# Kernel tuning notes

Hardware: AMD Instinct MI355X
Metric: run time of the kernel (lower is better)

## Reference

```python
import jax, jax.numpy as jnp
from jax import lax
import numpy as np

# ChannelMamba (bimamba_type='v2') from Wave-MambaAD VSSBlock.
# Dims: b=4, d_model=256 (channel dim of u), h=w=64 -> l=h*w=4096=dim,
# expand=1 -> d_inner=256, d_state=16, dt_rank=ceil(256/16)=16.
B_, DM, H_, W_ = 4, 256, 64, 64
L_ = H_ * W_            # == init arg `dim` (LayerNorm + depthwise-conv channels)
DI = DM                 # d_inner = expand * d_model
N_ = 16                 # d_state
R_ = 16                 # dt_rank


def setup_inputs() -> dict:
    key = jax.random.key(0)
    ks = jax.random.split(key, 12)
    s = 0.05
    # dt_proj bias init exactly as in the module: inv-softplus of dt in [1e-3, 1e-1]
    rs = np.random.RandomState(0)
    dt = np.exp(rs.rand(DI) * (np.log(0.1) - np.log(0.001)) + np.log(0.001))
    dt = np.clip(dt, 1e-4, None)
    inv_dt = dt + np.log1p(-np.exp(-dt))
    A_log = jnp.log(jnp.tile(jnp.arange(1, N_ + 1, dtype=jnp.float32), (DI, 1)))
    return {
        "u": jax.random.normal(ks[0], (B_, DM, H_, W_), jnp.float32),
        "in_proj_w": jax.random.normal(ks[1], (2 * DI, DM), jnp.float32) * s,
        "conv_w": jax.random.normal(ks[2], (L_, 1, 3, 3), jnp.float32) * s,  # depthwise, groups=L_
        "conv_b": jnp.zeros((L_,), jnp.float32),
        "x_proj_w": jax.random.normal(ks[3], (R_ + 2 * N_, DI), jnp.float32) * s,
        "dt_proj_w": jax.random.normal(ks[4], (DI, R_), jnp.float32) * (R_ ** -0.5),
        "dt_bias": jnp.asarray(inv_dt, jnp.float32),
        "A_log": A_log,
        "D": jnp.ones((DI,), jnp.float32),
        "x_proj_b_w": jax.random.normal(ks[5], (R_ + 2 * N_, DI), jnp.float32) * s,
        "dt_proj_b_w": jax.random.normal(ks[6], (DI, R_), jnp.float32) * (R_ ** -0.5),
        "A_b_log": A_log,
        "D_b": jnp.ones((DI,), jnp.float32),
        "ln_w": jnp.ones((L_,), jnp.float32),
        "ln_b": jnp.zeros((L_,), jnp.float32),
        "ln1_w": jnp.ones((L_,), jnp.float32),
        "ln1_b": jnp.zeros((L_,), jnp.float32),
    }


def _layernorm(x, w, b, eps=1e-5):
    m = jnp.mean(x, axis=-1, keepdims=True)
    v = jnp.mean(jnp.square(x - m), axis=-1, keepdims=True)
    return (x - m) * lax.rsqrt(v + eps) * w + b


def _selective_scan(u, delta, A, Bm, Cm, D, z, delta_bias):
    # u, delta, z: (b,d,l); A: (d,n); Bm, Cm: (b,n,l); D, delta_bias: (d,)
    delta = jax.nn.softplus(delta + delta_bias[None, :, None])
    dT = jnp.transpose(delta, (2, 0, 1))  # (l,b,d)
    uT = jnp.transpose(u, (2, 0, 1))      # (l,b,d)
    BT = jnp.transpose(Bm, (2, 0, 1))     # (l,b,n)
    CT = jnp.transpose(Cm, (2, 0, 1))     # (l,b,n)

    def step(hcar, inp):
        d_t, u_t, B_t, C_t = inp
        dA = jnp.exp(d_t[:, :, None] * A)                       # (b,d,n)
        hcar = hcar * dA + (d_t * u_t)[:, :, None] * B_t[:, None, :]
        y_t = jnp.einsum('bdn,bn->bd', hcar, C_t)
        return hcar, y_t

    h0 = jnp.zeros((u.shape[0], u.shape[1], A.shape[1]), u.dtype)
    _, ys = lax.scan(step, h0, (dT, uT, BT, CT))                 # ys: (l,b,d)
    y = jnp.transpose(ys, (1, 2, 0)) + D[None, :, None] * u      # (b,d,l)
    return y * jax.nn.silu(z)                                    # internal z-gate of selective_scan_fn


def reference(u, in_proj_w, conv_w, conv_b, x_proj_w, dt_proj_w, dt_bias, A_log, D,
              x_proj_b_w, dt_proj_b_w, A_b_log, D_b, ln_w, ln_b, ln1_w, ln1_b):
    b, d, h, w = u.shape
    l = h * w
    r = dt_proj_w.shape[1]
    n = A_log.shape[1]
    u_bld = u.reshape(b, d, l).transpose(0, 2, 1)                # (b,l,d)
    xz = jnp.einsum('ed,bld->bel', in_proj_w, u_bld)             # (b,2*d_inner,l), no bias
    x, z = jnp.split(xz, 2, axis=1)                              # each (b,d_inner,l)

    # depthwise 3x3 conv: channels = l, spatial = (1, d_inner), padding 1 (no activation!)
    xc = x.transpose(0, 2, 1)[:, :, None, :]                     # (b,l,1,d_inner)
    xc = lax.conv_general_dilated(xc, conv_w, (1, 1), ((1, 1), (1, 1)),
                                  feature_group_count=l,
                                  dimension_numbers=('NCHW', 'OIHW', 'NCHW'))
    x = (xc + conv_b[None, :, None, None])[:, :, 0, :].transpose(0, 2, 1)  # (b,d_inner,l)

    def proj(xp_w, dtp_w):
        dbl = jnp.einsum('kd,bdl->bkl', xp_w, x)                 # (b,r+2n,l)
        dt = jnp.einsum('dr,brl->bdl', dtp_w, dbl[:, :r])        # (b,d_inner,l), no bias here
        return dt, dbl[:, r:r + n], dbl[:, r + n:]               # dt, B, C

    A = -jnp.exp(A_log)
    A_b = -jnp.exp(A_b_log)
    dt, Bm, Cm = proj(x_proj_w, dt_proj_w)
    dtb, Bb, Cb = proj(x_proj_b_w, dt_proj_b_w)

    y = _selective_scan(x, dt, A, Bm, Cm, D, z, dt_bias)
    # backward scan: flipped input; NOTE: module uses forward dt_bias and unflipped z here
    yb = _selective_scan(x[:, :, ::-1], dtb, A_b, Bb, Cb, D_b, z, dt_bias)

    out = _layernorm(y, ln_w, ln_b) * jax.nn.silu(z)
    out_b = _layernorm(yb, ln1_w, ln1_b) * jax.nn.silu(z)
    return (out + out_b[:, :, ::-1]).reshape(b, d, h, w)
```

## Files before the change

kernel.cpp:

```cpp
#include <hip/hip_runtime.h>
#include <math.h>

#define BN 4
#define DD 256
#define LL 4096
#define NS 16
#define NCH 128
#define CT 32
#define SROW 36
#define BROW 20
#define LOG2E 1.4426950408889634f

typedef __bf16 bf16x8 __attribute__((ext_vector_type(8)));
typedef float f32x4 __attribute__((ext_vector_type(4)));

__device__ __forceinline__ float softplus_f(float v) {
  float e = __builtin_amdgcn_exp2f(v * LOG2E);
  float r = 0.69314718056f * __builtin_amdgcn_logf(1.f + e);
  return v > 20.f ? v : r;
}
__device__ __forceinline__ float silu_f(float v) {
  return v / (1.f + __expf(-v));
}
__device__ __forceinline__ f32x4 exp2v(f32x4 a) {
  f32x4 r;
  r[0] = __builtin_amdgcn_exp2f(a[0]);
  r[1] = __builtin_amdgcn_exp2f(a[1]);
  r[2] = __builtin_amdgcn_exp2f(a[2]);
  r[3] = __builtin_amdgcn_exp2f(a[3]);
  return r;
}

__global__ __launch_bounds__(256) void k1_mfma(
    const float* __restrict__ W, const float* __restrict__ u,
    float* __restrict__ xpre, float* __restrict__ zb) {
  __shared__ float Af[128 * 36];
  __shared__ float Bf[32 * 68];
  const int l0 = blockIdx.x * 64;
  const int e0 = blockIdx.y * 128;
  const int b  = blockIdx.z;
  const int tid = threadIdx.x;
  const int lane = tid & 63, w = tid >> 6;
  const int m16 = lane & 15, quad = lane >> 4;

  f32x4 acc[2][4];
#pragma unroll
  for (int i = 0; i < 2; ++i)
#pragma unroll
    for (int j = 0; j < 4; ++j) acc[i][j] = (f32x4){0.f, 0.f, 0.f, 0.f};

  const float* Ub = u + (size_t)b * DD * LL;

  for (int k0 = 0; k0 < DD; k0 += 32) {
    if (k0) __syncthreads();
#pragma unroll
    for (int it = 0; it < 4; ++it) {
      int f4 = tid + it * 256;
      int e = f4 >> 3, kq = f4 & 7;
      *(float4*)&Af[e * 36 + kq * 4] =
          *(const float4*)(W + (size_t)(e0 + e) * DD + k0 + kq * 4);
    }
#pragma unroll
    for (int it = 0; it < 2; ++it) {
      int f4 = tid + it * 256;
      int kk = f4 >> 4, lq = f4 & 15;
      *(float4*)&Bf[kk * 68 + lq * 4] =
          *(const float4*)(Ub + (size_t)(k0 + kk) * LL + l0 + lq * 4);
    }
    __syncthreads();
    bf16x8 afr[2], bfr[4];
#pragma unroll
    for (int te = 0; te < 2; ++te) {
      const float* src = &Af[(w * 32 + te * 16 + m16) * 36 + quad * 8];
      bf16x8 t;
#pragma unroll
      for (int j = 0; j < 8; ++j) t[j] = (__bf16)src[j];
      afr[te] = t;
    }
#pragma unroll
    for (int tl = 0; tl < 4; ++tl) {
      bf16x8 t;
#pragma unroll
      for (int j = 0; j < 8; ++j) t[j] = (__bf16)Bf[(quad * 8 + j) * 68 + tl * 16 + m16];
      bfr[tl] = t;
    }
#pragma unroll
    for (int te = 0; te < 2; ++te)
#pragma unroll
      for (int tl = 0; tl < 4; ++tl)
        acc[te][tl] = __builtin_amdgcn_mfma_f32_16x16x32_bf16(afr[te], bfr[tl], acc[te][tl], 0, 0, 0);
  }

#pragma unroll
  for (int te = 0; te < 2; ++te) {
#pragma unroll
    for (int tl = 0; tl < 4; ++tl) {
      int col = l0 + tl * 16 + m16;
#pragma unroll
      for (int r = 0; r < 4; ++r) {
        int e = e0 + w * 32 + te * 16 + quad * 4 + r;
        float v = acc[te][tl][r];
        if (e < DD) xpre[((size_t)b * DD + e) * LL + col] = v;
        else        zb[((size_t)b * DD + (e - DD)) * LL + col] = v;
      }
    }
  }
}

__global__ __launch_bounds__(256) void k2_conv(
    const float* __restrict__ xpre, const float* __restrict__ cw,
    const float* __restrict__ cb, float* __restrict__ xo) {
  const int bd = blockIdx.x;
  const int d = bd & 255;
  const size_t row = (size_t)bd * LL;
  const float* r1 = xpre + row;
  const bool has0 = d > 0, has2 = d < DD - 1;
  for (int j = threadIdx.x; j < LL; j += 256) {
    float w0 = cw[j * 9 + 3], w1 = cw[j * 9 + 4], w2 = cw[j * 9 + 5];
    float v = cb[j] + r1[j] * w1;
    if (has0) v += r1[j - LL] * w0;
    if (has2) v += r1[j + LL] * w2;
    xo[row + j] = v;
  }
}

__global__ __launch_bounds__(256) void k3_xproj(
    const float* __restrict__ xc,
    const float* __restrict__ xpw, const float* __restrict__ xpwB,
    float* __restrict__ dtr, float* __restrict__ gB, float* __restrict__ gC) {
  const int tid = threadIdx.x;
  const int l   = blockIdx.x * 256 + tid;
  const int b   = blockIdx.y;
  const int zz  = blockIdx.z;
  const int dir = zz >> 3, rg = zz & 7;
  const int rbase = rg * 6;
  const float* W = (dir ? xpwB : xpw) + (size_t)rbase * DD;
  const float* xcol = xc + (size_t)b * DD * LL + l;

  float acc[6] = {0.f, 0.f, 0.f, 0.f, 0.f, 0.f};

#pragma unroll 8
  for (int d = 0; d < DD; ++d) {
    float xv = xcol[(size_t)d * LL];
#pragma unroll
    for (int i = 0; i < 6; ++i) acc[i] += W[i * DD + d] * xv;
  }

  const size_t ob = ((size_t)dir * BN + b);
#pragma unroll
  for (int i = 0; i < 6; ++i) {
    int r = rbase + i;
    if (r < 16)
      dtr[(ob * 16 + r) * LL + l] = acc[i];
    else if (r < 32)
      gB[(ob * NS + (r - 16)) * LL + l] = acc[i];
    else
      gC[(ob * NS + (r - 32)) * LL + l] = acc[i];
  }
}

__global__ __launch_bounds__(256) void k3b_dtproj(
    const float* __restrict__ dtr,
    const float* __restrict__ dtw, const float* __restrict__ dtwB,
    const float* __restrict__ dtb,
    float* __restrict__ gdelta) {
  const int tid = threadIdx.x;
  const int l   = blockIdx.x * 256 + tid;
  const int b   = blockIdx.y & 3;
  const int dir = blockIdx.y >> 2;
  const int d0  = blockIdx.z * 16;
  const size_t ob = ((size_t)dir * BN + b);
  const float* dw = (dir ? dtwB : dtw);

  float tr[16];
#pragma unroll
  for (int r = 0; r < 16; ++r) tr[r] = dtr[(ob * 16 + r) * LL + l];

#pragma unroll
  for (int d = d0; d < d0 + 16; ++d) {
    float acc = dtb[d];
#pragma unroll
    for (int r = 0; r < 16; ++r) acc += dw[d * 16 + r] * tr[r];
    gdelta[(ob * DD + d) * LL + l] = softplus_f(acc);
  }
}

__global__ __launch_bounds__(256) void k4_scanA(
    const float* __restrict__ gdelta, const float* __restrict__ x,
    const float* __restrict__ gB,
    const float* __restrict__ Alog, const float* __restrict__ AlogB,
    float* __restrict__ Pbuf, float* __restrict__ qbuf) {
  __shared__ float sdl[64 * SROW];
  __shared__ float sx[64 * SROW];
  __shared__ float sB[CT * BROW];
  const int s = blockIdx.x;
  const int d0 = blockIdx.y * 64;
  const int dir = blockIdx.z >> 2, b = blockIdx.z & 3;
  const int t0 = s * CT;
  const int tid = threadIdx.x;
  const size_t ob = (size_t)dir * BN + b;

  {
    const int q = tid & 7, r2 = tid >> 3;
#pragma unroll
    for (int p = 0; p < 2; ++p) {
      int row = r2 + p * 32;
      f32x4 dl = *(const f32x4*)(gdelta + (ob * DD + d0 + row) * LL + t0 + q * 4);
      f32x4 xv;
      if (dir == 0) {
        xv = *(const f32x4*)(x + ((size_t)b * DD + d0 + row) * LL + t0 + q * 4);
      } else {
        f32x4 t = *(const f32x4*)(x + ((size_t)b * DD + d0 + row) * LL + (LL - 4 - t0 - q * 4));
        xv = (f32x4){t[3], t[2], t[1], t[0]};
      }
      *(f32x4*)&sdl[row * SROW + q * 4] = dl;
      *(f32x4*)&sx[row * SROW + q * 4] = xv;
    }
    const int t = tid & 31, n8 = tid >> 5;
#pragma unroll
    for (int p = 0; p < 2; ++p) {
      int n = n8 + p * 8;
      sB[t * BROW + n] = gB[(ob * NS + n) * LL + t0 + t];
    }
  }
  __syncthreads();

  const int dq = tid >> 2, sub = tid & 3, n0 = sub * 4;
  const int d = d0 + dq;
  f32x4 Al = *(const f32x4*)((dir ? AlogB : Alog) + d * NS + n0);
  f32x4 An2;
  An2[0] = -__expf(Al[0]) * LOG2E;
  An2[1] = -__expf(Al[1]) * LOG2E;
  An2[2] = -__expf(Al[2]) * LOG2E;
  An2[3] = -__expf(Al[3]) * LOG2E;

  f32x4 h = (f32x4){0.f, 0.f, 0.f, 0.f};
  float S = 0.f;

  for (int jb = 0; jb < CT; jb += 4) {
    f32x4 dl4 = *(const f32x4*)&sdl[dq * SROW + jb];
    f32x4 x4  = *(const f32x4*)&sx[dq * SROW + jb];
#pragma unroll
    for (int q = 0; q < 4; ++q) {
      int t = jb + q;
      f32x4 Bv = *(const f32x4*)&sB[t * BROW + n0];
      float dl = dl4[q];
      float dlx = dl * x4[q];
      f32x4 e = exp2v(dl * An2);
      h = h * e + dlx * Bv;
      S += dl;
    }
  }

  const size_t pidx = ((ob * DD + d) * (size_t)NCH + s) * NS + n0;
  *(f32x4*)(Pbuf + pidx) = exp2v(An2 * S);
  *(f32x4*)(qbuf + pidx) = h;
}

__global__ __launch_bounds__(64) void k5_mid(
    const float* __restrict__ Pbuf, float* __restrict__ qbuf) {
  int id = blockIdx.x * 64 + threadIdx.x;
  int n = id & 15;
  int d = (id >> 4) & 255;
  int rb = id >> 12;
  size_t base = (((size_t)rb * DD + d) * NCH) * NS + n;
  float h = 0.f;
  for (int s0 = 0; s0 < NCH; s0 += 8) {
    float Pv[8], qv[8];
#pragma unroll
    for (int k = 0; k < 8; ++k) {
      size_t idx = base + (size_t)(s0 + k) * NS;
      Pv[k] = Pbuf[idx];
      qv[k] = qbuf[idx];
    }
#pragma unroll
    for (int k = 0; k < 8; ++k) {
      size_t idx = base + (size_t)(s0 + k) * NS;
      qbuf[idx] = h;
      h = h * Pv[k] + qv[k];
    }
  }
}

__global__ __launch_bounds__(256) void k6_scanC(
    const float* __restrict__ gdelta, const float* __restrict__ x,
    const float* __restrict__ gB, const float* __restrict__ gC,
    const float* __restrict__ zb,
    const float* __restrict__ Alog, const float* __restrict__ AlogB,
    const float* __restrict__ Dvec, const float* __restrict__ DvecB,
    const float* __restrict__ hstart,
    float* __restrict__ y, float* __restrict__ yb) {
  __shared__ float sdl[64 * SROW];
  __shared__ float sx[64 * SROW];
  __shared__ float sB[CT * BROW];
  __shared__ float sC[CT * BROW];
  __shared__ float ylds[64 * 36];
  __shared__ float sD[64];
  const int s = blockIdx.x;
  const int d0 = blockIdx.y * 64;
  const int dir = blockIdx.z >> 2, b = blockIdx.z & 3;
  const int t0 = s * CT;
  const int tid = threadIdx.x;
  const size_t ob = (size_t)dir * BN + b;

  {
    const int q = tid & 7, r2 = tid >> 3;
#pragma unroll
    for (int p = 0; p < 2; ++p) {
      int row = r2 + p * 32;
      f32x4 dl = *(const f32x4*)(gdelta + (ob * DD + d0 + row) * LL + t0 + q * 4);
      f32x4 xv;
      if (dir == 0) {
        xv = *(const f32x4*)(x + ((size_t)b * DD + d0 + row) * LL + t0 + q * 4);
      } else {
        f32x4 t = *(const f32x4*)(x + ((size_t)b * DD + d0 + row) * LL + (LL - 4 - t0 - q * 4));
        xv = (f32x4){t[3], t[2], t[1], t[0]};
      }
      *(f32x4*)&sdl[row * SROW + q * 4] = dl;
      *(f32x4*)&sx[row * SROW + q * 4] = xv;
    }
    const int t = tid & 31, n8 = tid >> 5;
#pragma unroll
    for (int p = 0; p < 2; ++p) {
      int n = n8 + p * 8;
      sB[t * BROW + n] = gB[(ob * NS + n) * LL + t0 + t];
      sC[t * BROW + n] = gC[(ob * NS + n) * LL + t0 + t];
    }
    if (tid < 64) sD[tid] = (dir ? DvecB : Dvec)[d0 + tid];
  }
  __syncthreads();

  const int dq = tid >> 2, sub = tid & 3, n0 = sub * 4;
  const int lane = tid & 63, w = tid >> 6;
  const int d = d0 + dq;
  f32x4 Al = *(const f32x4*)((dir ? AlogB : Alog) + d * NS + n0);
  f32x4 An2;
  An2[0] = -__expf(Al[0]) * LOG2E;
  An2[1] = -__expf(Al[1]) * LOG2E;
  An2[2] = -__expf(Al[2]) * LOG2E;
  An2[3] = -__expf(Al[3]) * LOG2E;

  const size_t pidx = ((ob * DD + d) * (size_t)NCH + s) * NS + n0;
  f32x4 h = *(const f32x4*)(hstart + pidx);

  const float* zbase = zb + ((size_t)b * DD + d0) * LL + t0;
  float* dbase = (dir ? yb : y) + ((size_t)b * DD + d0) * LL + t0;
  const int dql = lane >> 3, tql = lane & 7;

  for (int jb = 0; jb < CT; jb += 8) {
#pragma unroll
    for (int j2 = 0; j2 < 8; j2 += 4) {
      f32x4 dl4 = *(const f32x4*)&sdl[dq * SROW + jb + j2];
      f32x4 x4  = *(const f32x4*)&sx[dq * SROW + jb + j2];
#pragma unroll
      for (int q = 0; q < 4; ++q) {
        int t = jb + j2 + q;
        f32x4 Bv = *(const f32x4*)&sB[t * BROW + n0];
        f32x4 Cv = *(const f32x4*)&sC[t * BROW + n0];
        float dl = dl4[q];
        float dlx = dl * x4[q];
        f32x4 e = exp2v(dl * An2);
        h = h * e + dlx * Bv;
        f32x4 yc = h * Cv;
        ylds[dq * 36 + ((j2 + q) << 2) + sub] = (yc[0] + yc[1]) + (yc[2] + yc[3]);
      }
    }
#pragma unroll
    for (int k = 0; k < 2; ++k) {
      int dd = w * 16 + dql + 8 * k;
      int tt = jb + tql;
      f32x4 pv = *(const f32x4*)&ylds[dd * 36 + tql * 4];
      float sum = (pv[0] + pv[1]) + (pv[2] + pv[3]);
      float xv = sx[dd * SROW + tt];
      float zv = zbase[(size_t)dd * LL + tt];
      dbase[(size_t)dd * LL + tt] = (sum + sD[dd] * xv) * silu_f(zv);
    }
  }
}

__global__ __launch_bounds__(256) void k7_final(
    const float* __restrict__ y, const float* __restrict__ yb,
    const float* __restrict__ zb,
    const float* __restrict__ lnw, const float* __restrict__ lnb,
    const float* __restrict__ ln1w, const float* __restrict__ ln1b,
    float* __restrict__ out) {
  __shared__ float sy[LL];
  __shared__ float syb[LL];
  __shared__ float rsum[4][4];
  const int row = blockIdx.x;
  const int tid = threadIdx.x;
  const size_t base = (size_t)row * LL;
  float s1y = 0.f, s2y = 0.f, s1b = 0.f, s2b = 0.f;
  for (int j = tid * 4; j < LL; j += 1024) {
    float4 v = *(const float4*)(y + base + j);
    *(float4*)&sy[j] = v;
    s1y += v.x + v.y + v.z + v.w;
    s2y += v.x * v.x + v.y * v.y + v.z * v.z + v.w * v.w;
    float4 w = *(const float4*)(yb + base + j);
    *(float4*)&syb[j] = w;
    s1b += w.x + w.y + w.z + w.w;
    s2b += w.x * w.x + w.y * w.y + w.z * w.z + w.w * w.w;
  }
#pragma unroll
  for (int m = 1; m < 64; m <<= 1) {
    s1y += __shfl_xor(s1y, m); s2y += __shfl_xor(s2y, m);
    s1b += __shfl_xor(s1b, m); s2b += __shfl_xor(s2b, m);
  }
  int wv = tid >> 6;
  if ((tid & 63) == 0) { rsum[wv][0] = s1y; rsum[wv][1] = s2y; rsum[wv][2] = s1b; rsum[wv][3] = s2b; }
  __syncthreads();
  float t1y = rsum[0][0] + rsum[1][0] + rsum[2][0] + rsum[3][0];
  float t2y = rsum[0][1] + rsum[1][1] + rsum[2][1] + rsum[3][1];
  float t1b = rsum[0][2] + rsum[1][2] + rsum[2][2] + rsum[3][2];
  float t2b = rsum[0][3] + rsum[1][3] + rsum[2][3] + rsum[3][3];
  const float inv = 1.f / (float)LL;
  float mY = t1y * inv; float vY = t2y * inv - mY * mY; float rY = rsqrtf(vY + 1e-5f);
  float mB = t1b * inv; float vB = t2b * inv - mB * mB; float rB = rsqrtf(vB + 1e-5f);
  for (int j = tid; j < LL; j += 256) {
    int jr = LL - 1 - j;
    float a  = (sy[j]  - mY) * rY * lnw[j]   + lnb[j];
    float g1 = silu_f(zb[base + j]);
    float bv = (syb[jr] - mB) * rB * ln1w[jr] + ln1b[jr];
    float g2 = silu_f(zb[base + jr]);
    out[base + j] = a * g1 + bv * g2;
  }
}

extern "C" void kernel_launch(void* const* d_in, const int* in_sizes, int n_in,
                              void* d_out, int out_size, void* d_ws, size_t ws_size,
                              hipStream_t stream) {
  const float* u     = (const float*)d_in[0];
  const float* inw   = (const float*)d_in[1];
  const float* cw    = (const float*)d_in[2];
  const float* cb    = (const float*)d_in[3];
  const float* xpw   = (const float*)d_in[4];
  const float* dtw   = (const float*)d_in[5];
  const float* dtb   = (const float*)d_in[6];
  const float* Alog  = (const float*)d_in[7];
  const float* Dv    = (const float*)d_in[8];
  const float* xpwB  = (const float*)d_in[9];
  const float* dtwB  = (const float*)d_in[10];
  const float* AlogB = (const float*)d_in[11];
  const float* DvB   = (const float*)d_in[12];
  const float* lnw   = (const float*)d_in[13];
  const float* lnb   = (const float*)d_in[14];
  const float* ln1w  = (const float*)d_in[15];
  const float* ln1b  = (const float*)d_in[16];
  float* out = (float*)d_out;

  float* ws = (float*)d_ws;
  const size_t SZ = (size_t)BN * DD * LL;
  float* xpre   = ws;
  float* zb     = ws + SZ;
  float* xc     = ws + 2 * SZ;
  float* gdelta = ws + 3 * SZ;
  float* gB     = ws + 5 * SZ;
  float* gC     = gB + SZ / 8;
  float* Pbuf   = gC + SZ / 8;
  float* qbuf   = Pbuf + SZ;
  float* ybuf   = xpre;
  float* ybbuf  = Pbuf;
  float* dtr    = Pbuf;

  k1_mfma<<<dim3(64, 4, 4), 256, 0, stream>>>(inw, u, xpre, zb);
  k2_conv<<<1024, 256, 0, stream>>>(xpre, cw, cb, xc);
  k3_xproj<<<dim3(16, 4, 16), 256, 0, stream>>>(xc, xpw, xpwB, dtr, gB, gC);
  k3b_dtproj<<<dim3(16, 8, 16), 256, 0, stream>>>(dtr, dtw, dtwB, dtb, gdelta);
  k4_scanA<<<dim3(NCH - 1, 4, 8), 256, 0, stream>>>(gdelta, xc, gB, Alog, AlogB, Pbuf, qbuf);
  k5_mid<<<512, 64, 0, stream>>>(Pbuf, qbuf);
  k6_scanC<<<dim3(NCH, 4, 8), 256, 0, stream>>>(gdelta, xc, gB, gC, zb, Alog, AlogB,
                                                Dv, DvB, qbuf, ybuf, ybbuf);
  k7_final<<<1024, 256, 0, stream>>>(ybuf, ybbuf, zb, lnw, lnb, ln1w, ln1b, out);
}
```

Measured before the change: 245.3 us.

## Read scan inputs directly from global memory, store chunk delta sums, reduce via DPP

The chunked scan kernels no longer stage delta and x rows through shared memory. Each thread reads its own row straight from global memory, with the 4 threads of a quad reading the same addresses. Scan-A now writes one scalar delta sum per chunk instead of 16 decay factors, and the middle pass recomputes the decay with exp2. Scan-C replaces the LDS-based y reduction with a DPP quad reduction and has each thread write 8 contiguous outputs, which removes shared-memory traffic and barriers. The cost is redundant global/L1 loads across a quad and extra exp work in the middle pass.

New measurement: 259.5 us. +5.8%, slower.

```diff
diff --git a/kernel.cpp b/kernel.cpp
--- a/kernel.cpp
+++ b/kernel.cpp
@@ -7,7 +7,6 @@
 #define NS 16
 #define NCH 128
 #define CT 32
-#define SROW 36
 #define BROW 20
 #define LOG2E 1.4426950408889634f
 
@@ -29,6 +28,12 @@
   r[2] = __builtin_amdgcn_exp2f(a[2]);
   r[3] = __builtin_amdgcn_exp2f(a[3]);
   return r;
+}
+__device__ __forceinline__ float quad_reduce(float v) {
+  int t = __builtin_amdgcn_mov_dpp(__float_as_int(v), 0xB1, 0xF, 0xF, true);
+  v += __int_as_float(t);
+  t = __builtin_amdgcn_mov_dpp(__float_as_int(v), 0x4E, 0xF, 0xF, true);
+  return v + __int_as_float(t);
 }
 
 __global__ __launch_bounds__(256) void k1_mfma(
@@ -189,10 +194,8 @@
     const float* __restrict__ gdelta, const float* __restrict__ x,
     const float* __restrict__ gB,
     const float* __restrict__ Alog, const float* __restrict__ AlogB,
-    float* __restrict__ Pbuf, float* __restrict__ qbuf) {
-  __shared__ float sdl[64 * SROW];
-  __shared__ float sx[64 * SROW];
-  __shared__ float sB[CT * BROW];
+    float* __restrict__ Sbuf, float* __restrict__ qbuf) {
+  __shared__ __align__(16) float sB[CT * BROW];
   const int s = blockIdx.x;
   const int d0 = blockIdx.y * 64;
   const int dir = blockIdx.z >> 2, b = blockIdx.z & 3;
@@ -201,21 +204,6 @@
   const size_t ob = (size_t)dir * BN + b;
 
   {
-    const int q = tid & 7, r2 = tid >> 3;
-#pragma unroll
-    for (int p = 0; p < 2; ++p) {
-      int row = r2 + p * 32;
-      f32x4 dl = *(const f32x4*)(gdelta + (ob * DD + d0 + row) * LL + t0 + q * 4);
-      f32x4 xv;
-      if (dir == 0) {
-        xv = *(const f32x4*)(x + ((size_t)b * DD + d0 + row) * LL + t0 + q * 4);
-      } else {
-        f32x4 t = *(const f32x4*)(x + ((size_t)b * DD + d0 + row) * LL + (LL - 4 - t0 - q * 4));
-        xv = (f32x4){t[3], t[2], t[1], t[0]};
-      }
-      *(f32x4*)&sdl[row * SROW + q * 4] = dl;
-      *(f32x4*)&sx[row * SROW + q * 4] = xv;
-    }
     const int t = tid & 31, n8 = tid >> 5;
 #pragma unroll
     for (int p = 0; p < 2; ++p) {
@@ -234,12 +222,21 @@
   An2[2] = -__expf(Al[2]) * LOG2E;
   An2[3] = -__expf(Al[3]) * LOG2E;
 
+  const float* dlrow = gdelta + (ob * DD + d) * LL + t0;
+  const float* xrow  = x + ((size_t)b * DD + d) * LL;
+
   f32x4 h = (f32x4){0.f, 0.f, 0.f, 0.f};
   float S = 0.f;
 
   for (int jb = 0; jb < CT; jb += 4) {
-    f32x4 dl4 = *(const f32x4*)&sdl[dq * SROW + jb];
-    f32x4 x4  = *(const f32x4*)&sx[dq * SROW + jb];
+    f32x4 dl4 = *(const f32x4*)(dlrow + jb);
+    f32x4 x4;
+    if (dir == 0) {
+      x4 = *(const f32x4*)(xrow + t0 + jb);
+    } else {
+      f32x4 t = *(const f32x4*)(xrow + (LL - 4 - t0 - jb));
+      x4 = (f32x4){t[3], t[2], t[1], t[0]};
+    }
 #pragma unroll
     for (int q = 0; q < 4; ++q) {
       int t = jb + q;
@@ -252,32 +249,36 @@
     }
   }
 
+  if (sub == 0) Sbuf[(ob * DD + d) * (size_t)NCH + s] = S;
   const size_t pidx = ((ob * DD + d) * (size_t)NCH + s) * NS + n0;
-  *(f32x4*)(Pbuf + pidx) = exp2v(An2 * S);
   *(f32x4*)(qbuf + pidx) = h;
 }
 
 __global__ __launch_bounds__(64) void k5_mid(
-    const float* __restrict__ Pbuf, float* __restrict__ qbuf) {
+    const float* __restrict__ Sbuf,
+    const float* __restrict__ Alog, const float* __restrict__ AlogB,
+    float* __restrict__ qbuf) {
   int id = blockIdx.x * 64 + threadIdx.x;
   int n = id & 15;
   int d = (id >> 4) & 255;
   int rb = id >> 12;
+  int dir = rb >> 2;
+  float An2 = -__expf((dir ? AlogB : Alog)[d * NS + n]) * LOG2E;
   size_t base = (((size_t)rb * DD + d) * NCH) * NS + n;
+  size_t sbase = ((size_t)rb * DD + d) * NCH;
   float h = 0.f;
   for (int s0 = 0; s0 < NCH; s0 += 8) {
-    float Pv[8], qv[8];
+    float Sv[8], qv[8];
 #pragma unroll
     for (int k = 0; k < 8; ++k) {
-      size_t idx = base + (size_t)(s0 + k) * NS;
-      Pv[k] = Pbuf[idx];
-      qv[k] = qbuf[idx];
+      Sv[k] = Sbuf[sbase + s0 + k];
+      qv[k] = qbuf[base + (size_t)(s0 + k) * NS];
     }
 #pragma unroll
     for (int k = 0; k < 8; ++k) {
       size_t idx = base + (size_t)(s0 + k) * NS;
       qbuf[idx] = h;
-      h = h * Pv[k] + qv[k];
+      h = h * __builtin_amdgcn_exp2f(An2 * Sv[k]) + qv[k];
     }
   }
 }
@@ -290,12 +291,8 @@
     const float* __restrict__ Dvec, const float* __restrict__ DvecB,
     const float* __restrict__ hstart,
     float* __restrict__ y, float* __restrict__ yb) {
-  __shared__ float sdl[64 * SROW];
-  __shared__ float sx[64 * SROW];
-  __shared__ float sB[CT * BROW];
-  __shared__ float sC[CT * BROW];
-  __shared__ float ylds[64 * 36];
-  __shared__ float sD[64];
+  __shared__ __align__(16) float sB[CT * BROW];
+  __shared__ __align__(16) float sC[CT * BROW];
   const int s = blockIdx.x;
   const int d0 = blockIdx.y * 64;
   const int dir = blockIdx.z >> 2, b = blockIdx.z & 3;
@@ -304,21 +301,6 @@
   const size_t ob = (size_t)dir * BN + b;
 
   {
-    const int q = tid & 7, r2 = tid >> 3;
-#pragma unroll
-    for (int p = 0; p < 2; ++p) {
-      int row = r2 + p * 32;
-      f32x4 dl = *(const f32x4*)(gdelta + (ob * DD + d0 + row) * LL + t0 + q * 4);
-      f32x4 xv;
-      if (dir == 0) {
-        xv = *(const f32x4*)(x + ((size_t)b * DD + d0 + row) * LL + t0 + q * 4);
-      } else {
-        f32x4 t = *(const f32x4*)(x + ((size_t)b * DD + d0 + row) * LL + (LL - 4 - t0 - q * 4));
-        xv = (f32x4){t[3], t[2], t[1], t[0]};
-      }
-      *(f32x4*)&sdl[row * SROW + q * 4] = dl;
-      *(f32x4*)&sx[row * SROW + q * 4] = xv;
-    }
     const int t = tid & 31, n8 = tid >> 5;
 #pragma unroll
     for (int p = 0; p < 2; ++p) {
@@ -326,12 +308,10 @@
       sB[t * BROW + n] = gB[(ob * NS + n) * LL + t0 + t];
       sC[t * BROW + n] = gC[(ob * NS + n) * LL + t0 + t];
     }
-    if (tid < 64) sD[tid] = (dir ? DvecB : Dvec)[d0 + tid];
   }
   __syncthreads();
 
   const int dq = tid >> 2, sub = tid & 3, n0 = sub * 4;
-  const int lane = tid & 63, w = tid >> 6;
   const int d = d0 + dq;
   f32x4 Al = *(const f32x4*)((dir ? AlogB : Alog) + d * NS + n0);
   f32x4 An2;
@@ -339,43 +319,60 @@
   An2[1] = -__expf(Al[1]) * LOG2E;
   An2[2] = -__expf(Al[2]) * LOG2E;
   An2[3] = -__expf(Al[3]) * LOG2E;
+  const float Dd = (dir ? DvecB : Dvec)[d];
 
   const size_t pidx = ((ob * DD + d) * (size_t)NCH + s) * NS + n0;
   f32x4 h = *(const f32x4*)(hstart + pidx);
 
-  const float* zbase = zb + ((size_t)b * DD + d0) * LL + t0;
-  float* dbase = (dir ? yb : y) + ((size_t)b * DD + d0) * LL + t0;
-  const int dql = lane >> 3, tql = lane & 7;
+  const float* dlrow = gdelta + (ob * DD + d) * LL + t0;
+  const float* xrow  = x + ((size_t)b * DD + d) * LL;
+
+  float yreg[8], xreg[8];
 
   for (int jb = 0; jb < CT; jb += 8) {
-#pragma unroll
-    for (int j2 = 0; j2 < 8; j2 += 4) {
-      f32x4 dl4 = *(const f32x4*)&sdl[dq * SROW + jb + j2];
-      f32x4 x4  = *(const f32x4*)&sx[dq * SROW + jb + j2];
-#pragma unroll
-      for (int q = 0; q < 4; ++q) {
-        int t = jb + j2 + q;
-        f32x4 Bv = *(const f32x4*)&sB[t * BROW + n0];
-        f32x4 Cv = *(const f32x4*)&sC[t * BROW + n0];
-        float dl = dl4[q];
-        float dlx = dl * x4[q];
-        f32x4 e = exp2v(dl * An2);
-        h = h * e + dlx * Bv;
-        f32x4 yc = h * Cv;
-        ylds[dq * 36 + ((j2 + q) << 2) + sub] = (yc[0] + yc[1]) + (yc[2] + yc[3]);
-      }
-    }
-#pragma unroll
-    for (int k = 0; k < 2; ++k) {
-      int dd = w * 16 + dql + 8 * k;
-      int tt = jb + tql;
-      f32x4 pv = *(const f32x4*)&ylds[dd * 36 + tql * 4];
-      float sum = (pv[0] + pv[1]) + (pv[2] + pv[3]);
-      float xv = sx[dd * SROW + tt];
-      float zv = zbase[(size_t)dd * LL + tt];
-      dbase[(size_t)dd * LL + tt] = (sum + sD[dd] * xv) * silu_f(zv);
-    }
-  }
+    f32x4 dlA = *(const f32x4*)(dlrow + jb);
+    f32x4 dlB = *(const f32x4*)(dlrow + jb + 4);
+    f32x4 xA, xB;
+    if (dir == 0) {
+      xA = *(const f32x4*)(xrow + t0 + jb);
+      xB = *(const f32x4*)(xrow + t0 + jb + 4);
+    } else {
+      f32x4 ta = *(const f32x4*)(xrow + (LL - 4 - t0 - jb));
+      f32x4 tb = *(const f32x4*)(xrow + (LL - 4 - t0 - (jb + 4)));
+      xA = (f32x4){ta[3], ta[2], ta[1], ta[0]};
+      xB = (f32x4){tb[3], tb[2], tb[1], tb[0]};
+    }
+    const bool own = (sub == (jb >> 3));
+#pragma unroll
+    for (int tl = 0; tl < 8; ++tl) {
+      float dl = tl < 4 ? dlA[tl & 3] : dlB[tl & 3];
+      float xv = tl < 4 ? xA[tl & 3] : xB[tl & 3];
+      int t = jb + tl;
+      f32x4 Bv = *(const f32x4*)&sB[t * BROW + n0];
+      f32x4 Cv = *(const f32x4*)&sC[t * BROW + n0];
+      float dlx = dl * xv;
+      f32x4 e = exp2v(dl * An2);
+      h = h * e + dlx * Bv;
+      f32x4 yc = h * Cv;
+      float part = (yc[0] + yc[1]) + (yc[2] + yc[3]);
+      float sum = quad_reduce(part);
+      yreg[tl] = own ? sum : yreg[tl];
+      xreg[tl] = own ? xv : xreg[tl];
+    }
+  }
+
+  const size_t rbase = ((size_t)b * DD + d) * LL + t0 + sub * 8;
+  f32x4 z0 = *(const f32x4*)(zb + rbase);
+  f32x4 z1 = *(const f32x4*)(zb + rbase + 4);
+  float* dst = (dir ? yb : y) + rbase;
+  f32x4 o0, o1;
+#pragma unroll
+  for (int i = 0; i < 4; ++i) {
+    o0[i] = (yreg[i] + Dd * xreg[i]) * silu_f(z0[i]);
+    o1[i] = (yreg[i + 4] + Dd * xreg[i + 4]) * silu_f(z1[i]);
+  }
+  *(f32x4*)dst = o0;
+  *(f32x4*)(dst + 4) = o1;
 }
 
 __global__ __launch_bounds__(256) void k7_final(
@@ -456,18 +453,19 @@
   float* gdelta = ws + 3 * SZ;
   float* gB     = ws + 5 * SZ;
   float* gC     = gB + SZ / 8;
-  float* Pbuf   = gC + SZ / 8;
-  float* qbuf   = Pbuf + SZ;
+  float* Pregion= gC + SZ / 8;
+  float* qbuf   = Pregion + SZ;
+  float* Sbuf   = Pregion;
   float* ybuf   = xpre;
-  float* ybbuf  = Pbuf;
-  float* dtr    = Pbuf;
+  float* ybbuf  = Pregion;
+  float* dtr    = Pregion;
 
   k1_mfma<<<dim3(64, 4, 4), 256, 0, stream>>>(inw, u, xpre, zb);
   k2_conv<<<1024, 256, 0, stream>>>(xpre, cw, cb, xc);
   k3_xproj<<<dim3(16, 4, 16), 256, 0, stream>>>(xc, xpw, xpwB, dtr, gB, gC);
   k3b_dtproj<<<dim3(16, 8, 16), 256, 0, stream>>>(dtr, dtw, dtwB, dtb, gdelta);
-  k4_scanA<<<dim3(NCH - 1, 4, 8), 256, 0, stream>>>(gdelta, xc, gB, Alog, AlogB, Pbuf, qbuf);
-  k5_mid<<<512, 64, 0, stream>>>(Pbuf, qbuf);
+  k4_scanA<<<dim3(NCH - 1, 4, 8), 256, 0, stream>>>(gdelta, xc, gB, Alog, AlogB, Sbuf, qbuf);
+  k5_mid<<<512, 64, 0, stream>>>(Sbuf, Alog, AlogB, qbuf);
   k6_scanC<<<dim3(NCH, 4, 8), 256, 0, stream>>>(gdelta, xc, gB, gC, zb, Alog, AlogB,
                                                 Dv, DvB, qbuf, ybuf, ybbuf);
   k7_final<<<1024, 256, 0, stream>>>(ybuf, ybbuf, zb, lnw, lnb, ln1w, ln1b, out);
```

## Keep scan inputs in registers and reduce outputs with DPP in k6

Applied to the files above, without the earlier changes.

The chunked scan-output kernel no longer stages delta and x through shared memory. Each thread loads its own 32-step row into registers, reduces the partial y across the four state-group lanes with DPP quad shuffles instead of an LDS transpose, and writes eight contiguous outputs as vector stores. This removes most LDS traffic and the ylds round trip, and turns the scattered z and y accesses into coalesced vector accesses. In exchange it raises register pressure, and the four lanes of a quad issue redundant loads of the same delta and x row.

New measurement: 253.6 us. +3.4%, slower.

```diff
diff --git a/kernel.cpp b/kernel.cpp
--- a/kernel.cpp
+++ b/kernel.cpp
@@ -29,6 +29,12 @@
   r[2] = __builtin_amdgcn_exp2f(a[2]);
   r[3] = __builtin_amdgcn_exp2f(a[3]);
   return r;
+}
+__device__ __forceinline__ float quad_reduce(float v) {
+  int t = __builtin_amdgcn_mov_dpp(__float_as_int(v), 0xB1, 0xF, 0xF, true);
+  v += __int_as_float(t);
+  t = __builtin_amdgcn_mov_dpp(__float_as_int(v), 0x4E, 0xF, 0xF, true);
+  return v + __int_as_float(t);
 }
 
 __global__ __launch_bounds__(256) void k1_mfma(
@@ -290,12 +296,8 @@
     const float* __restrict__ Dvec, const float* __restrict__ DvecB,
     const float* __restrict__ hstart,
     float* __restrict__ y, float* __restrict__ yb) {
-  __shared__ float sdl[64 * SROW];
-  __shared__ float sx[64 * SROW];
-  __shared__ float sB[CT * BROW];
-  __shared__ float sC[CT * BROW];
-  __shared__ float ylds[64 * 36];
-  __shared__ float sD[64];
+  __shared__ __align__(16) float sB[CT * BROW];
+  __shared__ __align__(16) float sC[CT * BROW];
   const int s = blockIdx.x;
   const int d0 = blockIdx.y * 64;
   const int dir = blockIdx.z >> 2, b = blockIdx.z & 3;
@@ -304,21 +306,6 @@
   const size_t ob = (size_t)dir * BN + b;
 
   {
-    const int q = tid & 7, r2 = tid >> 3;
-#pragma unroll
-    for (int p = 0; p < 2; ++p) {
-      int row = r2 + p * 32;
-      f32x4 dl = *(const f32x4*)(gdelta + (ob * DD + d0 + row) * LL + t0 + q * 4);
-      f32x4 xv;
-      if (dir == 0) {
-        xv = *(const f32x4*)(x + ((size_t)b * DD + d0 + row) * LL + t0 + q * 4);
-      } else {
-        f32x4 t = *(const f32x4*)(x + ((size_t)b * DD + d0 + row) * LL + (LL - 4 - t0 - q * 4));
-        xv = (f32x4){t[3], t[2], t[1], t[0]};
-      }
-      *(f32x4*)&sdl[row * SROW + q * 4] = dl;
-      *(f32x4*)&sx[row * SROW + q * 4] = xv;
-    }
     const int t = tid & 31, n8 = tid >> 5;
 #pragma unroll
     for (int p = 0; p < 2; ++p) {
@@ -326,56 +313,80 @@
       sB[t * BROW + n] = gB[(ob * NS + n) * LL + t0 + t];
       sC[t * BROW + n] = gC[(ob * NS + n) * LL + t0 + t];
     }
-    if (tid < 64) sD[tid] = (dir ? DvecB : Dvec)[d0 + tid];
-  }
-  __syncthreads();
+  }
 
   const int dq = tid >> 2, sub = tid & 3, n0 = sub * 4;
-  const int lane = tid & 63, w = tid >> 6;
   const int d = d0 + dq;
+  const float* dlrow = gdelta + (ob * DD + d) * LL + t0;
+  const float* xrow  = x + ((size_t)b * DD + d) * LL;
+
+  f32x4 dlv[8], xv[8];
+#pragma unroll
+  for (int i = 0; i < 8; ++i) {
+    dlv[i] = *(const f32x4*)(dlrow + i * 4);
+    if (dir == 0) {
+      xv[i] = *(const f32x4*)(xrow + t0 + i * 4);
+    } else {
+      f32x4 t = *(const f32x4*)(xrow + (LL - 4 - t0 - i * 4));
+      xv[i] = (f32x4){t[3], t[2], t[1], t[0]};
+    }
+  }
+  const size_t pidx = ((ob * DD + d) * (size_t)NCH + s) * NS + n0;
+  f32x4 h = *(const f32x4*)(hstart + pidx);
+
   f32x4 Al = *(const f32x4*)((dir ? AlogB : Alog) + d * NS + n0);
   f32x4 An2;
   An2[0] = -__expf(Al[0]) * LOG2E;
   An2[1] = -__expf(Al[1]) * LOG2E;
   An2[2] = -__expf(Al[2]) * LOG2E;
   An2[3] = -__expf(Al[3]) * LOG2E;
-
-  const size_t pidx = ((ob * DD + d) * (size_t)NCH + s) * NS + n0;
-  f32x4 h = *(const f32x4*)(hstart + pidx);
-
-  const float* zbase = zb + ((size_t)b * DD + d0) * LL + t0;
-  float* dbase = (dir ? yb : y) + ((size_t)b * DD + d0) * LL + t0;
-  const int dql = lane >> 3, tql = lane & 7;
-
+  const float Dd = (dir ? DvecB : Dvec)[d];
+
+  __syncthreads();
+
+  float yreg[8];
+#pragma unroll
   for (int jb = 0; jb < CT; jb += 8) {
-#pragma unroll
-    for (int j2 = 0; j2 < 8; j2 += 4) {
-      f32x4 dl4 = *(const f32x4*)&sdl[dq * SROW + jb + j2];
-      f32x4 x4  = *(const f32x4*)&sx[dq * SROW + jb + j2];
-#pragma unroll
-      for (int q = 0; q < 4; ++q) {
-        int t = jb + j2 + q;
-        f32x4 Bv = *(const f32x4*)&sB[t * BROW + n0];
-        f32x4 Cv = *(const f32x4*)&sC[t * BROW + n0];
-        float dl = dl4[q];
-        float dlx = dl * x4[q];
-        f32x4 e = exp2v(dl * An2);
-        h = h * e + dlx * Bv;
-        f32x4 yc = h * Cv;
-        ylds[dq * 36 + ((j2 + q) << 2) + sub] = (yc[0] + yc[1]) + (yc[2] + yc[3]);
-      }
-    }
-#pragma unroll
-    for (int k = 0; k < 2; ++k) {
-      int dd = w * 16 + dql + 8 * k;
-      int tt = jb + tql;
-      f32x4 pv = *(const f32x4*)&ylds[dd * 36 + tql * 4];
-      float sum = (pv[0] + pv[1]) + (pv[2] + pv[3]);
-      float xv = sx[dd * SROW + tt];
-      float zv = zbase[(size_t)dd * LL + tt];
-      dbase[(size_t)dd * LL + tt] = (sum + sD[dd] * xv) * silu_f(zv);
-    }
-  }
+    const bool own = (sub == (jb >> 3));
+#pragma unroll
+    for (int tl = 0; tl < 8; ++tl) {
+      int t = jb + tl;
+      float dl = dlv[t >> 2][t & 3];
+      float dlx = dl * xv[t >> 2][t & 3];
+      f32x4 Bv = *(const f32x4*)&sB[t * BROW + n0];
+      f32x4 Cv = *(const f32x4*)&sC[t * BROW + n0];
+      f32x4 e = exp2v(dl * An2);
+      h = h * e + dlx * Bv;
+      f32x4 yc = h * Cv;
+      float part = (yc[0] + yc[1]) + (yc[2] + yc[3]);
+      float sum = quad_reduce(part);
+      yreg[tl] = own ? sum : yreg[tl];
+    }
+  }
+
+  const int s8 = sub * 8;
+  const size_t rbase = ((size_t)b * DD + d) * LL + t0 + s8;
+  f32x4 z0 = *(const f32x4*)(zb + rbase);
+  f32x4 z1 = *(const f32x4*)(zb + rbase + 4);
+  f32x4 xo0, xo1;
+  if (dir == 0) {
+    xo0 = *(const f32x4*)(xrow + t0 + s8);
+    xo1 = *(const f32x4*)(xrow + t0 + s8 + 4);
+  } else {
+    f32x4 ta = *(const f32x4*)(xrow + (LL - 4 - t0 - s8));
+    f32x4 tb = *(const f32x4*)(xrow + (LL - 4 - t0 - (s8 + 4)));
+    xo0 = (f32x4){ta[3], ta[2], ta[1], ta[0]};
+    xo1 = (f32x4){tb[3], tb[2], tb[1], tb[0]};
+  }
+  float* dst = (dir ? yb : y) + rbase;
+  f32x4 o0, o1;
+#pragma unroll
+  for (int i = 0; i < 4; ++i) {
+    o0[i] = (yreg[i] + Dd * xo0[i]) * silu_f(z0[i]);
+    o1[i] = (yreg[i + 4] + Dd * xo1[i]) * silu_f(z1[i]);
+  }
+  *(f32x4*)dst = o0;
+  *(f32x4*)(dst + 4) = o1;
 }
 
 __global__ __launch_bounds__(256) void k7_final(
```
